# Kernel optimization log

Measured on AMD Instinct MI355X. Metric: run time of the kernel, lower is better.

Reference implementation:

```python
import jax, jax.numpy as jnp
import numpy as np

NUM_EMBEDDINGS = 1024
EMBEDDING_DIM = 64
COMMITMENT_COST = 0.25


def setup_inputs() -> dict:
    key = jax.random.key(0)
    k1, k2 = jax.random.split(key)
    z = jax.random.normal(k1, (32, 32, 32, EMBEDDING_DIM), dtype=jnp.float32)
    # embedding.weight.data.uniform_(-1/num_embeddings, 1/num_embeddings)
    lim = 1.0 / NUM_EMBEDDINGS
    codebook = jax.random.uniform(k2, (NUM_EMBEDDINGS, EMBEDDING_DIM),
                                  dtype=jnp.float32, minval=-lim, maxval=lim)
    return {"z": z, "codebook": codebook}


def reference(z, codebook):
    beta = COMMITMENT_COST
    zf = z.reshape(-1, EMBEDDING_DIM)                      # [N, D]
    # Squared euclidean distances (argmin is invariant to sqrt in torch.cdist)
    d2 = (jnp.sum(zf * zf, axis=1, keepdims=True)          # [N, 1]
          + jnp.sum(codebook * codebook, axis=1)[None, :]  # [1, K]
          - 2.0 * jnp.einsum('nd,kd->nk', zf, codebook))   # [N, K]
    encoding_indices = jnp.argmin(d2, axis=1)              # [N] int32
    z_q = codebook[encoding_indices].reshape(z.shape)      # [..., D]
    sg = jax.lax.stop_gradient
    loss = jnp.mean((sg(z_q) - z) ** 2) + beta * jnp.mean((z_q - sg(z)) ** 2)
    z_q_st = z + sg(z_q - z)                               # straight-through
    return (z_q_st, loss, encoding_indices)
```

## Files before the change

### kernel.cpp

```cpp
#include <hip/hip_runtime.h>
#include <stdint.h>

#define N_ROWS 32768
#define DIM 64
#define K_CODES 1024
#define ROWS_PER_BLOCK 128
#define THREADS 512
#define CHUNK 256
#define NCHUNK (K_CODES / CHUNK)
#define NBLOCKS (N_ROWS / ROWS_PER_BLOCK)
#define N_ELEMS (N_ROWS * DIM)
#define ZT_STRIDE 128
#define CT_STRIDE 256


__device__ __forceinline__ float bfbits(uint32_t b) { return __uint_as_float(b << 16); }
__device__ __forceinline__ float bf_lo(uint32_t u) { return __uint_as_float(u << 16); }
__device__ __forceinline__ float bf_hi(uint32_t u) { return __uint_as_float(u & 0xFFFF0000u); }

__device__ __forceinline__ float round_bf16(float f) {
  uint32_t u = __float_as_uint(f);
  uint32_t r = ((u + 0x7FFFu + ((u >> 16) & 1u)) >> 16) << 16;
  return __uint_as_float(r);
}

__device__ __forceinline__ int zcol(int row) {
  return ((row >> 3) << 2) + (((row >> 2) & 1) << 6) + (row & 3);
}

template <typename F>
__device__ __forceinline__ float np_sum64(F get) {
  float r0 = get(0), r1 = get(1), r2 = get(2), r3 = get(3);
  float r4 = get(4), r5 = get(5), r6 = get(6), r7 = get(7);
  for (int i = 8; i < 64; i += 8) {
    r0 = __fadd_rn(r0, get(i + 0)); r1 = __fadd_rn(r1, get(i + 1));
    r2 = __fadd_rn(r2, get(i + 2)); r3 = __fadd_rn(r3, get(i + 3));
    r4 = __fadd_rn(r4, get(i + 4)); r5 = __fadd_rn(r5, get(i + 5));
    r6 = __fadd_rn(r6, get(i + 6)); r7 = __fadd_rn(r7, get(i + 7));
  }
  return __fadd_rn(__fadd_rn(__fadd_rn(r0, r1), __fadd_rn(r2, r3)),
                   __fadd_rn(__fadd_rn(r4, r5), __fadd_rn(r6, r7)));
}

__global__ __launch_bounds__(THREADS, 1) void vq_kernel(
    const void* __restrict__ z, const void* __restrict__ cb,
    float* __restrict__ out, double* __restrict__ partials) {
  const int tid = threadIdx.x;

  __shared__ int s_cnt[2];
  __shared__ float zt[DIM][ZT_STRIDE];
  __shared__ float ct[DIM][CT_STRIDE];
  __shared__ float s_cc[K_CODES];
  __shared__ float s_zz[ROWS_PER_BLOCK];
  __shared__ float s_bestW[8][ROWS_PER_BLOCK];
  __shared__ int   s_kW[8][ROWS_PER_BLOCK];
  __shared__ int   s_win[ROWS_PER_BLOCK];
  __shared__ double s_loss[ROWS_PER_BLOCK];

  if (tid < 2) s_cnt[tid] = 0;
  __syncthreads();
  if (tid < 128) {
    uint32_t wc = ((const uint32_t*)cb)[(size_t)tid * 255];
    float vc = fabsf(bfbits(wc & 0xFFFFu));
    if (vc == 0.0f || (vc > 5.9e-8f && vc < 32.0f)) atomicAdd(&s_cnt[1], 1);
    uint32_t wz = ((const uint32_t*)z)[(size_t)tid * 8191];
    float vz = fabsf(bfbits(wz & 0xFFFFu));
    if (vz == 0.0f || (vz > 5.9e-8f && vz < 32.0f)) atomicAdd(&s_cnt[0], 1);
  }
  __syncthreads();
  const bool z_bf16  = s_cnt[0] >= 96;
  const bool cb_bf16 = s_cnt[1] >= 96;

  const int TR = tid & 15;
  const int TK = tid >> 4;
  const size_t row0 = (size_t)blockIdx.x * ROWS_PER_BLOCK;

  for (int kk = tid; kk < K_CODES; kk += THREADS) {
    float r0, r1, r2, r3, r4, r5, r6, r7;
    if (cb_bf16) {
      const uint4* cp = (const uint4*)((const uint16_t*)cb + (size_t)kk * DIM);
      uint4 u = cp[0];
      r0 = __fmul_rn(bf_lo(u.x), bf_lo(u.x)); r1 = __fmul_rn(bf_hi(u.x), bf_hi(u.x));
      r2 = __fmul_rn(bf_lo(u.y), bf_lo(u.y)); r3 = __fmul_rn(bf_hi(u.y), bf_hi(u.y));
      r4 = __fmul_rn(bf_lo(u.z), bf_lo(u.z)); r5 = __fmul_rn(bf_hi(u.z), bf_hi(u.z));
      r6 = __fmul_rn(bf_lo(u.w), bf_lo(u.w)); r7 = __fmul_rn(bf_hi(u.w), bf_hi(u.w));
      #pragma unroll
      for (int j = 1; j < 8; ++j) {
        u = cp[j];
        r0 = __fadd_rn(r0, __fmul_rn(bf_lo(u.x), bf_lo(u.x)));
        r1 = __fadd_rn(r1, __fmul_rn(bf_hi(u.x), bf_hi(u.x)));
        r2 = __fadd_rn(r2, __fmul_rn(bf_lo(u.y), bf_lo(u.y)));
        r3 = __fadd_rn(r3, __fmul_rn(bf_hi(u.y), bf_hi(u.y)));
        r4 = __fadd_rn(r4, __fmul_rn(bf_lo(u.z), bf_lo(u.z)));
        r5 = __fadd_rn(r5, __fmul_rn(bf_hi(u.z), bf_hi(u.z)));
        r6 = __fadd_rn(r6, __fmul_rn(bf_lo(u.w), bf_lo(u.w)));
        r7 = __fadd_rn(r7, __fmul_rn(bf_hi(u.w), bf_hi(u.w)));
      }
    } else {
      const float4* cp = (const float4*)((const float*)cb + (size_t)kk * DIM);
      float4 a = cp[0], b = cp[1];
      r0 = __fmul_rn(a.x, a.x); r1 = __fmul_rn(a.y, a.y);
      r2 = __fmul_rn(a.z, a.z); r3 = __fmul_rn(a.w, a.w);
      r4 = __fmul_rn(b.x, b.x); r5 = __fmul_rn(b.y, b.y);
      r6 = __fmul_rn(b.z, b.z); r7 = __fmul_rn(b.w, b.w);
      #pragma unroll
      for (int j = 1; j < 8; ++j) {
        a = cp[2 * j]; b = cp[2 * j + 1];
        r0 = __fadd_rn(r0, __fmul_rn(a.x, a.x));
        r1 = __fadd_rn(r1, __fmul_rn(a.y, a.y));
        r2 = __fadd_rn(r2, __fmul_rn(a.z, a.z));
        r3 = __fadd_rn(r3, __fmul_rn(a.w, a.w));
        r4 = __fadd_rn(r4, __fmul_rn(b.x, b.x));
        r5 = __fadd_rn(r5, __fmul_rn(b.y, b.y));
        r6 = __fadd_rn(r6, __fmul_rn(b.z, b.z));
        r7 = __fadd_rn(r7, __fmul_rn(b.w, b.w));
      }
    }
    s_cc[kk] = __fadd_rn(__fadd_rn(__fadd_rn(r0, r1), __fadd_rn(r2, r3)),
                         __fadd_rn(__fadd_rn(r4, r5), __fadd_rn(r6, r7)));
  }

  if (z_bf16) {
    const uint4* src = (const uint4*)((const uint16_t*)z + row0 * DIM);
    #pragma unroll
    for (int j = 0; j < 2; ++j) {
      int idx = tid + THREADS * j;
      int row = idx >> 3, d0 = (idx & 7) * 8;
      int col = zcol(row);
      uint4 u = src[idx];
      zt[d0 + 0][col] = bf_lo(u.x); zt[d0 + 1][col] = bf_hi(u.x);
      zt[d0 + 2][col] = bf_lo(u.y); zt[d0 + 3][col] = bf_hi(u.y);
      zt[d0 + 4][col] = bf_lo(u.z); zt[d0 + 5][col] = bf_hi(u.z);
      zt[d0 + 6][col] = bf_lo(u.w); zt[d0 + 7][col] = bf_hi(u.w);
    }
  } else {
    const float4* src = (const float4*)((const float*)z + row0 * DIM);
    #pragma unroll
    for (int j = 0; j < 4; ++j) {
      int idx = tid + THREADS * j;
      int row = idx >> 4, d0 = (idx & 15) * 4;
      int col = zcol(row);
      float4 v = src[idx];
      zt[d0 + 0][col] = v.x; zt[d0 + 1][col] = v.y;
      zt[d0 + 2][col] = v.z; zt[d0 + 3][col] = v.w;
    }
  }
  __syncthreads();

  if (tid < ROWS_PER_BLOCK) {
    const int c0 = zcol(tid);
    s_zz[tid] = np_sum64([&](int d) { float v = zt[d][c0]; return __fmul_rn(v, v); });
  }

  float best[8] = {3.4e38f, 3.4e38f, 3.4e38f, 3.4e38f,
                   3.4e38f, 3.4e38f, 3.4e38f, 3.4e38f};
  int bk[8] = {0, 0, 0, 0, 0, 0, 0, 0};
  float acc[8][8];
  #pragma unroll
  for (int ri = 0; ri < 8; ++ri)
    #pragma unroll
    for (int ki = 0; ki < 8; ++ki) acc[ri][ki] = 0.0f;

  for (int c = 0; c < NCHUNK; ++c) {
    __syncthreads();
    if (cb_bf16) {
      const uint4* src = (const uint4*)((const uint16_t*)cb + (size_t)c * CHUNK * DIM);
      #pragma unroll
      for (int j = 0; j < 4; ++j) {
        int idx = tid + THREADS * j;
        int kc = idx >> 3, d0 = (idx & 7) * 8;
        uint4 u = src[idx];
        ct[d0 + 0][kc] = bf_lo(u.x); ct[d0 + 1][kc] = bf_hi(u.x);
        ct[d0 + 2][kc] = bf_lo(u.y); ct[d0 + 3][kc] = bf_hi(u.y);
        ct[d0 + 4][kc] = bf_lo(u.z); ct[d0 + 5][kc] = bf_hi(u.z);
        ct[d0 + 6][kc] = bf_lo(u.w); ct[d0 + 7][kc] = bf_hi(u.w);
      }
    } else {
      const float4* src = (const float4*)((const float*)cb + (size_t)c * CHUNK * DIM);
      #pragma unroll
      for (int j = 0; j < 8; ++j) {
        int idx = tid + THREADS * j;
        int kc = idx >> 4, d0 = (idx & 15) * 4;
        float4 v = src[idx];
        ct[d0 + 0][kc] = v.x; ct[d0 + 1][kc] = v.y;
        ct[d0 + 2][kc] = v.z; ct[d0 + 3][kc] = v.w;
      }
    }
    __syncthreads();

    #pragma unroll 4
    for (int d = 0; d < DIM; ++d) {
      float4 zA = *(const float4*)&zt[d][TR * 4];
      float4 zB = *(const float4*)&zt[d][TR * 4 + 64];
      float4 cA = *(const float4*)&ct[d][TK * 8];
      float4 cB = *(const float4*)&ct[d][TK * 8 + 4];
      float zv[8] = {zA.x, zA.y, zA.z, zA.w, zB.x, zB.y, zB.z, zB.w};
      float cv[8] = {cA.x, cA.y, cA.z, cA.w, cB.x, cB.y, cB.z, cB.w};
      #pragma unroll
      for (int ri = 0; ri < 8; ++ri)
        #pragma unroll
        for (int ki = 0; ki < 8; ++ki)
          acc[ri][ki] = __fadd_rn(acc[ri][ki], __fmul_rn(zv[ri], cv[ki]));
    }

    #pragma unroll
    for (int ri = 0; ri < 8; ++ri) {
      const float zzr = s_zz[TR * 8 + ri];
      #pragma unroll
      for (int ki = 0; ki < 8; ++ki) {
        const int k = c * CHUNK + TK * 8 + ki;
        float e = __fsub_rn(__fadd_rn(zzr, s_cc[k]), __fmul_rn(2.0f, acc[ri][ki]));
        if (e < best[ri]) { best[ri] = e; bk[ri] = k; }
        acc[ri][ki] = 0.0f;
      }
    }
  }

  #pragma unroll
  for (int ri = 0; ri < 8; ++ri) {
    float v = best[ri]; int k = bk[ri];
    {
      float v2 = __shfl_xor(v, 16, 64); int k2 = __shfl_xor(k, 16, 64);
      if (v2 < v || (v2 == v && k2 < k)) { v = v2; k = k2; }
      v2 = __shfl_xor(v, 32, 64); k2 = __shfl_xor(k, 32, 64);
      if (v2 < v || (v2 == v && k2 < k)) { v = v2; k = k2; }
    }
    best[ri] = v; bk[ri] = k;
  }
  {
    const int lane = tid & 63, wv = tid >> 6;
    if (lane < 16) {
      #pragma unroll
      for (int ri = 0; ri < 8; ++ri) {
        s_bestW[wv][lane * 8 + ri] = best[ri];
        s_kW[wv][lane * 8 + ri] = bk[ri];
      }
    }
  }
  __syncthreads();

  if (tid < ROWS_PER_BLOCK) {
    float b = 3.4e38f;
    int bbk = 0x7FFFFFFF;
    #pragma unroll
    for (int p = 0; p < 8; ++p) {
      float v = s_bestW[p][tid];
      int vk = s_kW[p][tid];
      if (v < b || (v == b && vk < bbk)) { b = v; bbk = vk; }
    }
    s_win[tid] = bbk;
    const int c0 = zcol(tid);
    double acc2 = 0.0;
    if (cb_bf16) {
      const uint16_t* cp = (const uint16_t*)cb + (size_t)bbk * DIM;
      for (int d = 0; d < DIM; ++d) {
        double df = (double)zt[d][c0] - (double)bfbits((uint32_t)cp[d]);
        acc2 = fma(df, df, acc2);
      }
    } else {
      const float* cp = (const float*)cb + (size_t)bbk * DIM;
      for (int d = 0; d < DIM; ++d) {
        double df = (double)zt[d][c0] - (double)cp[d];
        acc2 = fma(df, df, acc2);
      }
    }
    s_loss[tid] = acc2;
    out[(size_t)N_ELEMS + 1 + row0 + tid] = round_bf16((float)bbk);
  }
  __syncthreads();

  const size_t base = row0 * DIM;
  #pragma unroll
  for (int j = 0; j < 16; ++j) {
    int idx = tid + THREADS * j;
    int rr = idx >> 6, dd = idx & 63;
    int w = s_win[rr];
    float v;
    if (cb_bf16) v = bfbits((uint32_t)((const uint16_t*)cb)[(size_t)w * DIM + dd]);
    else         v = round_bf16(((const float*)cb)[(size_t)w * DIM + dd]);
    out[base + idx] = v;
  }

  if (tid == 0) {
    double s = 0.0;
    for (int i = 0; i < ROWS_PER_BLOCK; ++i) s += s_loss[i];
    partials[blockIdx.x] = s;
  }
}

__global__ __launch_bounds__(256) void vq_loss_kernel(
    const double* __restrict__ partials, float* __restrict__ out) {
  __shared__ double sh[256];
  const int tid = threadIdx.x;
  double s = 0.0;
  for (int i = tid; i < NBLOCKS; i += 256) s += partials[i];
  sh[tid] = s;
  __syncthreads();
  if (tid == 0) {
    double t = 0.0;
    for (int i = 0; i < 256; ++i) t += sh[i];
    out[N_ELEMS] = round_bf16((float)(1.25 * t / (double)N_ELEMS));
  }
}

extern "C" void kernel_launch(void* const* d_in, const int* in_sizes, int n_in,
                              void* d_out, int out_size, void* d_ws, size_t ws_size,
                              hipStream_t stream) {
  const void* z  = d_in[0];
  const void* cb = d_in[1];
  float* out = (float*)d_out;
  uint8_t* ws = (uint8_t*)d_ws;
  double* partials = (double*)(ws + 8192);

  vq_kernel<<<NBLOCKS, THREADS, 0, stream>>>(z, cb, out, partials);
  vq_loss_kernel<<<1, 256, 0, stream>>>(partials, out);
}
```

Baseline: 140.9 us.

## Swizzle shared-memory tiles and fuse loss reduction via last-block counter

XOR-swizzles the column index of the transposed z and codebook shared-memory tiles so the staging stores hit fewer LDS bank conflicts. Every read of those tiles (matmul loop, norms, loss) is updated to match. It also removes the separate loss-reduction kernel: each block bumps an atomic counter after writing its partial, and the last block sums all partials. This saves a kernel launch but adds a memset and a threadfence/atomic per block.

After: 137.3 us. -2.6%, faster.

```diff
diff --git a/kernel.cpp b/kernel.cpp
--- a/kernel.cpp
+++ b/kernel.cpp
@@ -44,10 +44,12 @@
 
 __global__ __launch_bounds__(THREADS, 1) void vq_kernel(
     const void* __restrict__ z, const void* __restrict__ cb,
-    float* __restrict__ out, double* __restrict__ partials) {
+    float* __restrict__ out, double* __restrict__ partials,
+    unsigned int* __restrict__ counter) {
   const int tid = threadIdx.x;
 
   __shared__ int s_cnt[2];
+  __shared__ int s_last;
   __shared__ float zt[DIM][ZT_STRIDE];
   __shared__ float ct[DIM][CT_STRIDE];
   __shared__ float s_cc[K_CODES];
@@ -125,8 +127,8 @@
     #pragma unroll
     for (int j = 0; j < 2; ++j) {
       int idx = tid + THREADS * j;
-      int row = idx >> 3, d0 = (idx & 7) * 8;
-      int col = zcol(row);
+      int row = idx >> 3, w = idx & 7, d0 = w * 8;
+      int col = zcol(row) ^ (w << 2);
       uint4 u = src[idx];
       zt[d0 + 0][col] = bf_lo(u.x); zt[d0 + 1][col] = bf_hi(u.x);
       zt[d0 + 2][col] = bf_lo(u.y); zt[d0 + 3][col] = bf_hi(u.y);
@@ -139,7 +141,7 @@
     for (int j = 0; j < 4; ++j) {
       int idx = tid + THREADS * j;
       int row = idx >> 4, d0 = (idx & 15) * 4;
-      int col = zcol(row);
+      int col = zcol(row) ^ (((d0 >> 3) & 7) << 2);
       float4 v = src[idx];
       zt[d0 + 0][col] = v.x; zt[d0 + 1][col] = v.y;
       zt[d0 + 2][col] = v.z; zt[d0 + 3][col] = v.w;
@@ -149,7 +151,9 @@
 
   if (tid < ROWS_PER_BLOCK) {
     const int c0 = zcol(tid);
-    s_zz[tid] = np_sum64([&](int d) { float v = zt[d][c0]; return __fmul_rn(v, v); });
+    s_zz[tid] = np_sum64([&](int d) {
+      float v = zt[d][c0 ^ (((d >> 3) & 7) << 2)];
+      return __fmul_rn(v, v); });
   }
 
   float best[8] = {3.4e38f, 3.4e38f, 3.4e38f, 3.4e38f,
@@ -168,12 +172,13 @@
       #pragma unroll
       for (int j = 0; j < 4; ++j) {
         int idx = tid + THREADS * j;
-        int kc = idx >> 3, d0 = (idx & 7) * 8;
+        int kc = idx >> 3, w = idx & 7, d0 = w * 8;
+        int col = kc ^ ((w & 3) << 3);
         uint4 u = src[idx];
-        ct[d0 + 0][kc] = bf_lo(u.x); ct[d0 + 1][kc] = bf_hi(u.x);
-        ct[d0 + 2][kc] = bf_lo(u.y); ct[d0 + 3][kc] = bf_hi(u.y);
-        ct[d0 + 4][kc] = bf_lo(u.z); ct[d0 + 5][kc] = bf_hi(u.z);
-        ct[d0 + 6][kc] = bf_lo(u.w); ct[d0 + 7][kc] = bf_hi(u.w);
+        ct[d0 + 0][col] = bf_lo(u.x); ct[d0 + 1][col] = bf_hi(u.x);
+        ct[d0 + 2][col] = bf_lo(u.y); ct[d0 + 3][col] = bf_hi(u.y);
+        ct[d0 + 4][col] = bf_lo(u.z); ct[d0 + 5][col] = bf_hi(u.z);
+        ct[d0 + 6][col] = bf_lo(u.w); ct[d0 + 7][col] = bf_hi(u.w);
       }
     } else {
       const float4* src = (const float4*)((const float*)cb + (size_t)c * CHUNK * DIM);
@@ -181,19 +186,22 @@
       for (int j = 0; j < 8; ++j) {
         int idx = tid + THREADS * j;
         int kc = idx >> 4, d0 = (idx & 15) * 4;
+        int col = kc ^ (((d0 >> 3) & 3) << 3);
         float4 v = src[idx];
-        ct[d0 + 0][kc] = v.x; ct[d0 + 1][kc] = v.y;
-        ct[d0 + 2][kc] = v.z; ct[d0 + 3][kc] = v.w;
+        ct[d0 + 0][col] = v.x; ct[d0 + 1][col] = v.y;
+        ct[d0 + 2][col] = v.z; ct[d0 + 3][col] = v.w;
       }
     }
     __syncthreads();
 
     #pragma unroll 4
     for (int d = 0; d < DIM; ++d) {
-      float4 zA = *(const float4*)&zt[d][TR * 4];
-      float4 zB = *(const float4*)&zt[d][TR * 4 + 64];
-      float4 cA = *(const float4*)&ct[d][TK * 8];
-      float4 cB = *(const float4*)&ct[d][TK * 8 + 4];
+      const int zs = ((d >> 3) & 7) << 2;
+      const int cs = ((d >> 3) & 3) << 3;
+      float4 zA = *(const float4*)&zt[d][(TR << 2) ^ zs];
+      float4 zB = *(const float4*)&zt[d][((TR << 2) ^ zs) + 64];
+      float4 cA = *(const float4*)&ct[d][(TK << 3) ^ cs];
+      float4 cB = *(const float4*)&ct[d][((TK << 3) ^ cs) + 4];
       float zv[8] = {zA.x, zA.y, zA.z, zA.w, zB.x, zB.y, zB.z, zB.w};
       float cv[8] = {cA.x, cA.y, cA.z, cA.w, cB.x, cB.y, cB.z, cB.w};
       #pragma unroll
@@ -254,13 +262,14 @@
     if (cb_bf16) {
       const uint16_t* cp = (const uint16_t*)cb + (size_t)bbk * DIM;
       for (int d = 0; d < DIM; ++d) {
-        double df = (double)zt[d][c0] - (double)bfbits((uint32_t)cp[d]);
+        double df = (double)zt[d][c0 ^ (((d >> 3) & 7) << 2)]
+                  - (double)bfbits((uint32_t)cp[d]);
         acc2 = fma(df, df, acc2);
       }
     } else {
       const float* cp = (const float*)cb + (size_t)bbk * DIM;
       for (int d = 0; d < DIM; ++d) {
-        double df = (double)zt[d][c0] - (double)cp[d];
+        double df = (double)zt[d][c0 ^ (((d >> 3) & 7) << 2)] - (double)cp[d];
         acc2 = fma(df, df, acc2);
       }
     }
@@ -285,21 +294,20 @@
     double s = 0.0;
     for (int i = 0; i < ROWS_PER_BLOCK; ++i) s += s_loss[i];
     partials[blockIdx.x] = s;
-  }
-}
-
-__global__ __launch_bounds__(256) void vq_loss_kernel(
-    const double* __restrict__ partials, float* __restrict__ out) {
-  __shared__ double sh[256];
-  const int tid = threadIdx.x;
-  double s = 0.0;
-  for (int i = tid; i < NBLOCKS; i += 256) s += partials[i];
-  sh[tid] = s;
-  __syncthreads();
-  if (tid == 0) {
-    double t = 0.0;
-    for (int i = 0; i < 256; ++i) t += sh[i];
-    out[N_ELEMS] = round_bf16((float)(1.25 * t / (double)N_ELEMS));
+    __threadfence();
+    unsigned int old = atomicAdd(counter, 1u);
+    s_last = (old == NBLOCKS - 1) ? 1 : 0;
+  }
+  __syncthreads();
+  if (s_last) {
+    __threadfence();
+    if (tid < 128) s_loss[tid] = partials[tid] + partials[tid + 128];
+    __syncthreads();
+    if (tid == 0) {
+      double t = 0.0;
+      for (int i = 0; i < 128; ++i) t += s_loss[i];
+      out[N_ELEMS] = round_bf16((float)(1.25 * t / (double)N_ELEMS));
+    }
   }
 }
 
@@ -310,8 +318,9 @@
   const void* cb = d_in[1];
   float* out = (float*)d_out;
   uint8_t* ws = (uint8_t*)d_ws;
+  unsigned int* counter = (unsigned int*)(ws + 4096);
   double* partials = (double*)(ws + 8192);
 
-  vq_kernel<<<NBLOCKS, THREADS, 0, stream>>>(z, cb, out, partials);
-  vq_loss_kernel<<<1, 256, 0, stream>>>(partials, out);
-}
+  hipMemsetAsync(counter, 0, 4, stream);
+  vq_kernel<<<NBLOCKS, THREADS, 0, stream>>>(z, cb, out, partials, counter);
+}
```
